# Performance work log

Measured on AMD Instinct MI355X. Metric: run time of the kernel, lower is better.

Reference implementation:

```python
import jax, jax.numpy as jnp
import numpy as np

N_NODES = 50000
N_EDGES = 800000
DIM = 128
HEADS = 8
DK = DIM // HEADS  # 16
SQRT_DK = float(np.sqrt(DK))


def setup_inputs() -> dict:
    key = jax.random.key(0)
    ks = jax.random.split(key, 12)
    inp = {
        "h": jax.random.normal(ks[0], (N_NODES, DIM), jnp.float32),
        "src": jax.random.randint(ks[1], (N_EDGES,), 0, N_NODES, jnp.int32),
        "dst": jax.random.randint(ks[2], (N_EDGES,), 0, N_NODES, jnp.int32),
        "Wk": jax.random.normal(ks[3], (DIM, DIM), jnp.float32) / np.sqrt(DIM),
        "bk": jnp.zeros((DIM,), jnp.float32),
        "Wq": jax.random.normal(ks[4], (DIM, DIM), jnp.float32) / np.sqrt(DIM),
        "bq": jnp.zeros((DIM,), jnp.float32),
        "Wv": jax.random.normal(ks[5], (DIM, DIM), jnp.float32) / np.sqrt(DIM),
        "bv": jnp.zeros((DIM,), jnp.float32),
        "Wa": jax.random.normal(ks[6], (DIM, DIM), jnp.float32) / np.sqrt(DIM),
        "ba": jnp.zeros((DIM,), jnp.float32),
        "rel_att": jax.random.normal(ks[7], (HEADS, DK, DK), jnp.float32) / np.sqrt(DK),
        "rel_msg": jax.random.normal(ks[8], (HEADS, DK, DK), jnp.float32) / np.sqrt(DK),
        "rel_pri": jnp.ones((HEADS,), jnp.float32),
        "skip": jnp.ones((1,), jnp.float32),
    }
    return inp


def reference(h, src, dst, Wk, bk, Wq, bq, Wv, bv, Wa, ba, rel_att, rel_msg, rel_pri, skip):
    N = h.shape[0]
    # node-level projections -> [N, H, d_k]
    k = (h @ Wk + bk).reshape(N, HEADS, DK)
    q = (h @ Wq + bq).reshape(N, HEADS, DK)
    v = (h @ Wv + bv).reshape(N, HEADS, DK)
    # relation-specific transforms
    k = jnp.einsum('nhi,hij->nhj', k, rel_att)
    v = jnp.einsum('nhi,hij->nhj', v, rel_msg)
    # per-edge score: dot(q[dst], k[src]) over d_k -> [E, H]
    score = jnp.einsum('ehd,ehd->eh', q[dst], k[src]) * rel_pri / SQRT_DK
    # segment softmax over destination nodes (edge_softmax, norm_by='dst')
    smax = jax.ops.segment_max(score, dst, num_segments=N)  # [N, H]
    e = jnp.exp(score - smax[dst])
    ssum = jax.ops.segment_sum(e, dst, num_segments=N)  # [N, H]
    attn = e / ssum[dst]  # [E, H]
    # weighted scatter-sum of messages: sum_e v[src_e] * attn_e -> [N, H, d_k]
    m = v[src] * attn[:, :, None]
    t = jax.ops.segment_sum(m, dst, num_segments=N).reshape(N, DIM)
    # target-specific aggregation (dropout in eval mode = identity, use_norm=False)
    trans_out = t @ Wa + ba
    alpha = jax.nn.sigmoid(skip)  # [1], broadcasts
    new_h = trans_out * alpha + h * (1.0 - alpha)
    return new_h
```

## Files before the change

### kernel.cpp

```cpp
#include <hip/hip_runtime.h>
#include <stdint.h>

#define NN 50000
#define NE 800000

typedef __bf16 v8bf __attribute__((ext_vector_type(8)));
typedef float  v4f  __attribute__((ext_vector_type(4)));
typedef unsigned short v8us __attribute__((ext_vector_type(8)));

#define EXP2F(x) __builtin_amdgcn_exp2f(x)

__device__ __forceinline__ float bf2f(unsigned short u) {
    return __uint_as_float(((unsigned)u) << 16);
}
__device__ __forceinline__ unsigned short f2bf(float f) {
    unsigned u = __float_as_uint(f);
    u += 0x7FFFu + ((u >> 16) & 1u);
    return (unsigned short)(u >> 16);
}
__device__ __forceinline__ float ldf(const void* p, size_t i, int isb) {
    return isb ? bf2f(((const unsigned short*)p)[i]) : ((const float*)p)[i];
}
__device__ __forceinline__ unsigned uminu(unsigned a, unsigned b) {
    return a < b ? a : b;
}
union bcast8 { v8us u; v8bf b; };

__global__ __launch_bounds__(128) void k_prep0(
    const void* __restrict__ Wq, const void* __restrict__ bq,
    const void* __restrict__ Wk, const void* __restrict__ bk,
    const void* __restrict__ Wv, const void* __restrict__ bv,
    const void* __restrict__ Wa, const void* __restrict__ ba,
    const void* __restrict__ rel_att, const void* __restrict__ rel_msg,
    const void* __restrict__ rel_pri,
    unsigned* __restrict__ CNTP,
    int* __restrict__ FLAG, unsigned short* __restrict__ WTb,
    float* __restrict__ BC)
{
    int b = blockIdx.x;
    int j = threadIdx.x;
    if (b >= 512) {
        unsigned idx = (unsigned)(b - 512) * 128u + (unsigned)j;
        uint4 z = make_uint4(0, 0, 0, 0);
        #pragma unroll
        for (int t = 0; t < 25; ++t) {
            unsigned o = idx + (unsigned)t * 8192u;
            if (o < 200004u) ((uint4*)CNTP)[o] = z;
        }
        return;
    }
    const unsigned rp0 = ((const unsigned*)rel_pri)[0];
    const int isb = ((rp0 & 0xFFFFu) != 0u) ? 1 : 0;
    int m = b >> 7;
    int i = b & 127;
    if (b == 0 && j == 0) FLAG[0] = isb;
    if (m == 0) {
        WTb[((size_t)(0 * 128 + j)) * 128 + i] = f2bf(ldf(Wq, i * 128 + j, isb));
        if (i == 0) BC[j] = ldf(bq, j, isb);
    } else if (m == 3) {
        WTb[((size_t)(3 * 128 + j)) * 128 + i] = f2bf(ldf(Wa, i * 128 + j, isb));
        if (i == 0) BC[3 * 128 + j] = ldf(ba, j, isb);
    } else {
        const void* W    = (m == 1) ? Wk : Wv;
        const void* bias = (m == 1) ? bk : bv;
        const void* R    = (m == 1) ? rel_att : rel_msg;
        int hh = j >> 4, jj = j & 15;
        float scale = (m == 1) ? ldf(rel_pri, hh, isb) * 0.25f : 1.0f;
        float acc = 0.f, bacc = 0.f;
        #pragma unroll
        for (int l = 0; l < 16; ++l) {
            float r = ldf(R, hh * 256 + l * 16 + jj, isb);
            acc  += ldf(W, i * 128 + hh * 16 + l, isb) * r;
            bacc += ldf(bias, hh * 16 + l, isb) * r;
        }
        WTb[((size_t)(m * 128 + j)) * 128 + i] = f2bf(acc * scale);
        if (i == 0) BC[m * 128 + j] = bacc * scale;
    }
}

#define NBG 782
#define NHB 3125
#define NSB 98
__global__ __launch_bounds__(256) void k_qkvh(
    const void* __restrict__ h, const unsigned short* __restrict__ WTb,
    const float* __restrict__ BC, const int* __restrict__ FLAG,
    unsigned short* __restrict__ Qb, unsigned short* __restrict__ KVb,
    const int* __restrict__ dst,
    unsigned* __restrict__ CNTP, unsigned short* __restrict__ RANKS)
{
    __shared__ __align__(16) unsigned short Ah[64][136];
    const int tid = threadIdx.x;

    if (blockIdx.x >= NBG) {
        int e = (blockIdx.x - NBG) * 256 + tid;
        unsigned r = atomicAdd(&CNTP[(unsigned)dst[e] << 4], 1u);
        RANKS[e] = (unsigned short)r;
        return;
    }

    const int isb = FLAG[0];
    const int rowBase = blockIdx.x * 64;

    if (isb) {
        #pragma unroll
        for (int i = 0; i < 4; ++i) {
            int lin = tid + i * 256;
            int row = lin >> 4, kc = (lin & 15) * 8;
            int gr = rowBase + row;
            uint4 u = make_uint4(0, 0, 0, 0);
            if (gr < NN) u = *(const uint4*)((const unsigned short*)h + (size_t)gr * 128 + kc);
            *(uint4*)&Ah[row][kc] = u;
        }
    } else {
        #pragma unroll
        for (int i = 0; i < 8; ++i) {
            int lin = tid + i * 256;
            int row = lin >> 5, c4 = (lin & 31) * 4;
            int gr = rowBase + row;
            ushort4 o = make_ushort4(0, 0, 0, 0);
            if (gr < NN) {
                float4 f = *(const float4*)((const float*)h + (size_t)gr * 128 + c4);
                o.x = f2bf(f.x); o.y = f2bf(f.y); o.z = f2bf(f.z); o.w = f2bf(f.w);
            }
            *(ushort4*)&Ah[row][c4] = o;
        }
    }
    __syncthreads();

    const int w = tid >> 6, l = tid & 63;
    const int lr = l & 15, q = l >> 4;

    v8bf a[4];
    #pragma unroll
    for (int kk = 0; kk < 4; ++kk)
        a[kk] = *(const v8bf*)&Ah[w * 16 + lr][kk * 32 + q * 8];

    for (int m = 0; m < 3; ++m) {
        v4f acc[8];
        #pragma unroll
        for (int nt = 0; nt < 8; ++nt) {
            float bj = BC[m * 128 + nt * 16 + lr];
            acc[nt] = (v4f){bj, bj, bj, bj};
        }
        #pragma unroll
        for (int kk = 0; kk < 4; ++kk) {
            #pragma unroll
            for (int nt = 0; nt < 8; ++nt) {
                bcast8 bb;
                bb.u = *(const v8us*)(WTb + ((size_t)(m * 128 + nt * 16 + lr)) * 128
                                      + kk * 32 + q * 8);
                acc[nt] = __builtin_amdgcn_mfma_f32_16x16x32_bf16(a[kk], bb.b, acc[nt], 0, 0, 0);
            }
        }
        if (m == 0) {
            #pragma unroll
            for (int nt = 0; nt < 8; ++nt)
                #pragma unroll
                for (int r = 0; r < 4; ++r) {
                    int row = rowBase + w * 16 + q * 4 + r;
                    if (row < NN)
                        Qb[(size_t)row * 128 + nt * 16 + lr] = f2bf(acc[nt][r]);
                }
        } else {
            int ch = m - 1;
            #pragma unroll
            for (int nt = 0; nt < 8; ++nt)
                #pragma unroll
                for (int r = 0; r < 4; ++r) {
                    int row = rowBase + w * 16 + q * 4 + r;
                    if (row < NN)
                        KVb[(size_t)row * 256 + (nt * 16 + lr) * 2 + ch] = f2bf(acc[nt][r]);
                }
        }
    }
}

__global__ __launch_bounds__(256) void k_scan(
    const unsigned* __restrict__ CNTP,
    unsigned* __restrict__ RPS, unsigned* __restrict__ BSUM,
    unsigned* __restrict__ BOFF, unsigned* __restrict__ DONE)
{
    __shared__ unsigned shs[256];
    __shared__ int lastFlag;
    const int tid = threadIdx.x;
    int sb = blockIdx.x;
    int g0 = sb * 512 + tid * 2, g1 = g0 + 1;
    unsigned v0 = (g0 < NN) ? CNTP[(size_t)g0 << 4] : 0u;
    unsigned v1 = (g1 < NN) ? CNTP[(size_t)g1 << 4] : 0u;
    unsigned pv = v0 + v1;
    shs[tid] = pv;
    __syncthreads();
    #pragma unroll
    for (int off = 1; off < 256; off <<= 1) {
        unsigned t = 0;
        if (tid >= off) t = shs[tid - off];
        __syncthreads();
        if (tid >= off) shs[tid] += t;
        __syncthreads();
    }
    unsigned excl = shs[tid] - pv;
    if (g0 < NN) RPS[g0] = excl;
    if (g1 < NN) RPS[g1] = excl + v0;
    if (tid == 255) atomicExch(&BSUM[sb], shs[255]);
    __syncthreads();
    if (tid == 0) {
        __threadfence();
        lastFlag = (atomicAdd(DONE, 1u) == NSB - 1);
    }
    __syncthreads();
    if (!lastFlag) return;
    unsigned bv = (tid < NSB) ? atomicAdd(&BSUM[tid], 0u) : 0u;
    __syncthreads();
    shs[tid] = bv;
    __syncthreads();
    #pragma unroll
    for (int off = 1; off < 256; off <<= 1) {
        unsigned t = 0;
        if (tid >= off) t = shs[tid - off];
        __syncthreads();
        if (tid >= off) shs[tid] += t;
        __syncthreads();
    }
    if (tid < NSB) BOFF[tid] = shs[tid] - bv;
}

__global__ __launch_bounds__(256) void k_fill(
    const int* __restrict__ src, const int* __restrict__ dst,
    const unsigned short* __restrict__ RANKS,
    const unsigned* __restrict__ RPS, const unsigned* __restrict__ BOFF,
    unsigned short* __restrict__ ESRC, unsigned* __restrict__ ROW)
{
    int t = blockIdx.x * 256 + threadIdx.x;
    if (t < NN) ROW[t] = RPS[t] + BOFF[t >> 9];
    if (t >= NE / 2) return;
    int e = t * 2;
    const int2 d2 = *(const int2*)(dst + e);
    const int2 s2 = *(const int2*)(src + e);
    const ushort2 r2 = *(const ushort2*)(RANKS + e);
    unsigned p0 = RPS[d2.x] + BOFF[d2.x >> 9] + r2.x;
    unsigned p1 = RPS[d2.y] + BOFF[d2.y >> 9] + r2.y;
    ESRC[p0] = (unsigned short)s2.x;
    ESRC[p1] = (unsigned short)s2.y;
}

__global__ __launch_bounds__(256) void k_attn(
    const unsigned* __restrict__ ROW,
    const unsigned short* __restrict__ ESRC,
    const unsigned short* __restrict__ Qb, const unsigned short* __restrict__ KVb,
    unsigned short* __restrict__ Tb)
{
    int d = (blockIdx.x * 256 + threadIdx.x) >> 6;
    int lane = threadIdx.x & 63;
    int hl = lane >> 5;
    int sub = lane & 31;
    const float LOG2E = 1.4426950408889634f;

    unsigned beg = ROW[d];
    unsigned end = (d == NN - 1) ? (unsigned)NE : ROW[d + 1];

    const ushort4 qu = *(const ushort4*)(Qb + (size_t)d * 128 + sub * 4);
    float q0 = bf2f(qu.x) * LOG2E, q1 = bf2f(qu.y) * LOG2E;
    float q2 = bf2f(qu.z) * LOG2E, q3 = bf2f(qu.w) * LOG2E;

    float s = 0.f, o0 = 0.f, o1 = 0.f, o2 = 0.f, o3 = 0.f;
    int n = (int)(end - beg);

#define ATT_F(kv) {                                                         \
        float p = q0 * bf2f(kv[0]) + q1 * bf2f(kv[2])                       \
                + q2 * bf2f(kv[4]) + q3 * bf2f(kv[6]);                      \
        p += __shfl_xor(p, 1);                                              \
        p += __shfl_xor(p, 2);                                              \
        float wgt = EXP2F(p);                                               \
        s  += wgt;                                                          \
        o0 += wgt * bf2f(kv[1]); o1 += wgt * bf2f(kv[3]);                   \
        o2 += wgt * bf2f(kv[5]); o3 += wgt * bf2f(kv[7]); }
#define ATT_T(kv, idx) {                                                    \
        float p = q0 * bf2f(kv[0]) + q1 * bf2f(kv[2])                       \
                + q2 * bf2f(kv[4]) + q3 * bf2f(kv[6]);                      \
        p += __shfl_xor(p, 1);                                              \
        p += __shfl_xor(p, 2);                                              \
        float wgt = ((idx) < end) ? EXP2F(p) : 0.f;                         \
        s  += wgt;                                                          \
        o0 += wgt * bf2f(kv[1]); o1 += wgt * bf2f(kv[3]);                   \
        o2 += wgt * bf2f(kv[5]); o3 += wgt * bf2f(kv[7]); }
#define GATH(sid) (*(const v8us*)(KVB + (((unsigned)(sid) << 9) + voff)))

    if (n > 0) {
        const unsigned char* KVB = (const unsigned char*)KVb;
        const unsigned voff = (unsigned)(sub * 16);
        const unsigned last = end - 1;
        const int RT = (n + 7) >> 3;
        const int tail = n & 7;
        const unsigned b0 = beg + (unsigned)hl;

        unsigned sA0 = ESRC[uminu(b0 + 0u, last)];
        unsigned sA1 = ESRC[uminu(b0 + 2u, last)];
        unsigned sA2 = ESRC[uminu(b0 + 4u, last)];
        unsigned sA3 = ESRC[uminu(b0 + 6u, last)];
        v8us kA0 = GATH(sA0), kA1 = GATH(sA1), kA2 = GATH(sA2), kA3 = GATH(sA3);
        unsigned sB0 = 0, sB1 = 0, sB2 = 0, sB3 = 0;
        if (RT > 1) {
            unsigned b1 = b0 + 8u;
            sB0 = ESRC[uminu(b1 + 0u, last)];
            sB1 = ESRC[uminu(b1 + 2u, last)];
            sB2 = ESRC[uminu(b1 + 4u, last)];
            sB3 = ESRC[uminu(b1 + 6u, last)];
        }

        for (int r = 0; r < RT; ++r) {
            v8us kB0 = kA0, kB1 = kA1, kB2 = kA2, kB3 = kA3;
            if (r + 1 < RT) {
                kB0 = GATH(sB0); kB1 = GATH(sB1);
                kB2 = GATH(sB2); kB3 = GATH(sB3);
            }
            unsigned sC0 = sB0, sC1 = sB1, sC2 = sB2, sC3 = sB3;
            if (r + 2 < RT) {
                unsigned b2 = b0 + (unsigned)(8 * (r + 2));
                sC0 = ESRC[uminu(b2 + 0u, last)];
                sC1 = ESRC[uminu(b2 + 2u, last)];
                sC2 = ESRC[uminu(b2 + 4u, last)];
                sC3 = ESRC[uminu(b2 + 6u, last)];
            }
            if (r == RT - 1 && tail) {
                unsigned base = beg + (unsigned)(8 * r) + (unsigned)hl;
                ATT_T(kA0, base + 0u);
                ATT_T(kA1, base + 2u);
                ATT_T(kA2, base + 4u);
                ATT_T(kA3, base + 6u);
            } else {
                ATT_F(kA0); ATT_F(kA1); ATT_F(kA2); ATT_F(kA3);
            }
            kA0 = kB0; kA1 = kB1; kA2 = kB2; kA3 = kB3;
            sB0 = sC0; sB1 = sC1; sB2 = sC2; sB3 = sC3;
        }
    }
#undef ATT_F
#undef ATT_T
#undef GATH

    s  += __shfl_xor(s, 32);
    o0 += __shfl_xor(o0, 32);
    o1 += __shfl_xor(o1, 32);
    o2 += __shfl_xor(o2, 32);
    o3 += __shfl_xor(o3, 32);
    float r = (s > 0.f) ? (1.0f / s) : 0.f;
    if (hl == 0) {
        ushort4 o;
        o.x = f2bf(o0 * r); o.y = f2bf(o1 * r);
        o.z = f2bf(o2 * r); o.w = f2bf(o3 * r);
        *(ushort4*)(Tb + (size_t)d * 128 + sub * 4) = o;
    }
}

__global__ __launch_bounds__(256) void k_final_m(
    const unsigned short* __restrict__ Tb, const unsigned short* __restrict__ WTb,
    const float* __restrict__ BC, const void* __restrict__ h,
    const void* __restrict__ skip, const int* __restrict__ FLAG,
    void* __restrict__ out)
{
    __shared__ __align__(16) unsigned short Ah[64][136];
    const int isb = FLAG[0];
    const int tid = threadIdx.x;
    const int rowBase = blockIdx.x * 64;

    #pragma unroll
    for (int i = 0; i < 4; ++i) {
        int lin = tid + i * 256;
        int row = lin >> 4, kc = (lin & 15) * 8;
        int gr = rowBase + row;
        uint4 u = make_uint4(0, 0, 0, 0);
        if (gr < NN) u = *(const uint4*)(Tb + (size_t)gr * 128 + kc);
        *(uint4*)&Ah[row][kc] = u;
    }
    __syncthreads();

    const int w = tid >> 6, l = tid & 63;
    const int lr = l & 15, q = l >> 4;

    v8bf a[4];
    #pragma unroll
    for (int kk = 0; kk < 4; ++kk)
        a[kk] = *(const v8bf*)&Ah[w * 16 + lr][kk * 32 + q * 8];

    v4f acc[8];
    #pragma unroll
    for (int nt = 0; nt < 8; ++nt) {
        float bj = BC[3 * 128 + nt * 16 + lr];
        acc[nt] = (v4f){bj, bj, bj, bj};
    }
    #pragma unroll
    for (int kk = 0; kk < 4; ++kk) {
        #pragma unroll
        for (int nt = 0; nt < 8; ++nt) {
            bcast8 bb;
            bb.u = *(const v8us*)(WTb + ((size_t)(3 * 128 + nt * 16 + lr)) * 128
                                  + kk * 32 + q * 8);
            acc[nt] = __builtin_amdgcn_mfma_f32_16x16x32_bf16(a[kk], bb.b, acc[nt], 0, 0, 0);
        }
    }
    float skipv = ldf(skip, 0, isb);
    float alpha = 1.0f / (1.0f + __expf(-skipv));
    float beta = 1.0f - alpha;
    #pragma unroll
    for (int nt = 0; nt < 8; ++nt) {
        #pragma unroll
        for (int r = 0; r < 4; ++r) {
            int row = rowBase + w * 16 + q * 4 + r;
            if (row < NN) {
                size_t off = (size_t)row * 128 + nt * 16 + lr;
                float hv = ldf(h, off, isb);
                float o = alpha * acc[nt][r] + beta * hv;
                if (isb) ((unsigned short*)out)[off] = f2bf(o);
                else     ((float*)out)[off] = o;
            }
        }
    }
}

extern "C" void kernel_launch(void* const* d_in, const int* in_sizes, int n_in,
                              void* d_out, int out_size, void* d_ws, size_t ws_size,
                              hipStream_t stream)
{
    const void* h  = d_in[0];
    const int* src = (const int*)d_in[1];
    const int* dst = (const int*)d_in[2];
    const void* Wk = d_in[3];
    const void* bk = d_in[4];
    const void* Wq = d_in[5];
    const void* bq = d_in[6];
    const void* Wv = d_in[7];
    const void* bv = d_in[8];
    const void* Wa = d_in[9];
    const void* ba = d_in[10];
    const void* rel_att = d_in[11];
    const void* rel_msg = d_in[12];
    const void* rel_pri = d_in[13];
    const void* skip    = d_in[14];

    float* F = (float*)d_ws;
    int* FLAG      = (int*)F;
    float* BC      = F + 16;
    unsigned short* WTb = (unsigned short*)(BC + 512);
    unsigned* CNTP = (unsigned*)((float*)(BC + 512) + 32768);
    unsigned* DONE = CNTP + 800000;
    unsigned short* RANKS = (unsigned short*)(DONE + 16);
    unsigned* RPS  = (unsigned*)(RANKS + 800000);
    unsigned* BSUM = RPS + 50048;
    unsigned* BOFF = BSUM + 128;
    unsigned* ROW  = BOFF + 128;
    unsigned short* Tb = (unsigned short*)(ROW + 50048);
    unsigned short* ESRC = Tb + (size_t)NN * 128;
    unsigned short* Qb  = ESRC + NE;
    unsigned short* KVb = Qb + (size_t)NN * 128;

    k_prep0<<<512 + 64, 128, 0, stream>>>(Wq, bq, Wk, bk, Wv, bv, Wa, ba,
                                          rel_att, rel_msg, rel_pri,
                                          CNTP, FLAG, WTb, BC);
    k_qkvh<<<NBG + NHB, 256, 0, stream>>>(h, WTb, BC, FLAG, Qb, KVb,
                                          dst, CNTP, RANKS);
    k_scan<<<NSB, 256, 0, stream>>>(CNTP, RPS, BSUM, BOFF, DONE);
    k_fill<<<(NE / 2 + 255) / 256, 256, 0, stream>>>(src, dst, RANKS, RPS, BOFF, ESRC, ROW);
    k_attn<<<(NN * 64) / 256, 256, 0, stream>>>(ROW, ESRC, Qb, KVb, Tb);
    k_final_m<<<NBG, 256, 0, stream>>>(Tb, WTb, BC, h, skip, FLAG, d_out);
}
```

Before: 259.0 us.

## Split histogram from projection GEMM, vectorize dst loads and pack K/V stores

Moves the per-edge destination histogram and rank atomics out of the fused projection kernel into a separate launch. Each thread in the new launch handles four edges, loading dst as an int4 and writing ranks as a ushort4. The GEMM now keeps the K accumulators in registers and writes K and V together as one ushort2 store instead of two scattered 16-bit stores. The cost is an extra kernel launch and the loss of overlap between the atomic-heavy histogram and the MFMA GEMM. Holding K in registers also raises register pressure.

```diff
diff --git a/kernel.cpp b/kernel.cpp
--- a/kernel.cpp
+++ b/kernel.cpp
@@ -78,26 +78,33 @@
     }
 }
 
+__global__ __launch_bounds__(256) void k_hist(
+    const int* __restrict__ dst, unsigned* __restrict__ CNTP,
+    unsigned short* __restrict__ RANKS)
+{
+    int t = blockIdx.x * 256 + threadIdx.x;
+    if (t >= NE / 4) return;
+    int e = t * 4;
+    const int4 d4 = *(const int4*)(dst + e);
+    unsigned r0 = atomicAdd(&CNTP[(unsigned)d4.x << 4], 1u);
+    unsigned r1 = atomicAdd(&CNTP[(unsigned)d4.y << 4], 1u);
+    unsigned r2 = atomicAdd(&CNTP[(unsigned)d4.z << 4], 1u);
+    unsigned r3 = atomicAdd(&CNTP[(unsigned)d4.w << 4], 1u);
+    ushort4 r;
+    r.x = (unsigned short)r0; r.y = (unsigned short)r1;
+    r.z = (unsigned short)r2; r.w = (unsigned short)r3;
+    *(ushort4*)(RANKS + e) = r;
+}
+
 #define NBG 782
-#define NHB 3125
 #define NSB 98
-__global__ __launch_bounds__(256) void k_qkvh(
+__global__ __launch_bounds__(256) void k_gemm(
     const void* __restrict__ h, const unsigned short* __restrict__ WTb,
     const float* __restrict__ BC, const int* __restrict__ FLAG,
-    unsigned short* __restrict__ Qb, unsigned short* __restrict__ KVb,
-    const int* __restrict__ dst,
-    unsigned* __restrict__ CNTP, unsigned short* __restrict__ RANKS)
+    unsigned short* __restrict__ Qb, unsigned short* __restrict__ KVb)
 {
     __shared__ __align__(16) unsigned short Ah[64][136];
     const int tid = threadIdx.x;
-
-    if (blockIdx.x >= NBG) {
-        int e = (blockIdx.x - NBG) * 256 + tid;
-        unsigned r = atomicAdd(&CNTP[(unsigned)dst[e] << 4], 1u);
-        RANKS[e] = (unsigned short)r;
-        return;
-    }
-
     const int isb = FLAG[0];
     const int rowBase = blockIdx.x * 64;
 
@@ -135,6 +142,7 @@
     for (int kk = 0; kk < 4; ++kk)
         a[kk] = *(const v8bf*)&Ah[w * 16 + lr][kk * 32 + q * 8];
 
+    v4f accK[8];
     for (int m = 0; m < 3; ++m) {
         v4f acc[8];
         #pragma unroll
@@ -161,15 +169,21 @@
                     if (row < NN)
                         Qb[(size_t)row * 128 + nt * 16 + lr] = f2bf(acc[nt][r]);
                 }
+        } else if (m == 1) {
+            #pragma unroll
+            for (int nt = 0; nt < 8; ++nt) accK[nt] = acc[nt];
         } else {
-            int ch = m - 1;
             #pragma unroll
             for (int nt = 0; nt < 8; ++nt)
                 #pragma unroll
                 for (int r = 0; r < 4; ++r) {
                     int row = rowBase + w * 16 + q * 4 + r;
-                    if (row < NN)
-                        KVb[(size_t)row * 256 + (nt * 16 + lr) * 2 + ch] = f2bf(acc[nt][r]);
+                    if (row < NN) {
+                        ushort2 kv;
+                        kv.x = f2bf(accK[nt][r]);
+                        kv.y = f2bf(acc[nt][r]);
+                        *(ushort2*)&KVb[(size_t)row * 256 + (nt * 16 + lr) * 2] = kv;
+                    }
                 }
         }
     }
@@ -456,8 +470,8 @@
     k_prep0<<<512 + 64, 128, 0, stream>>>(Wq, bq, Wk, bk, Wv, bv, Wa, ba,
                                           rel_att, rel_msg, rel_pri,
                                           CNTP, FLAG, WTb, BC);
-    k_qkvh<<<NBG + NHB, 256, 0, stream>>>(h, WTb, BC, FLAG, Qb, KVb,
-                                          dst, CNTP, RANKS);
+    k_hist<<<(NE / 4 + 255) / 256, 256, 0, stream>>>(dst, CNTP, RANKS);
+    k_gemm<<<NBG, 256, 0, stream>>>(h, WTb, BC, FLAG, Qb, KVb);
     k_scan<<<NSB, 256, 0, stream>>>(CNTP, RPS, BSUM, BOFF, DONE);
     k_fill<<<(NE / 2 + 255) / 256, 256, 0, stream>>>(src, dst, RANKS, RPS, BOFF, ESRC, ROW);
     k_attn<<<(NN * 64) / 256, 256, 0, stream>>>(ROW, ESRC, Qb, KVb, Tb);
```

Measured after the change: 286.5 us. 10.6% more time.
